# Kernel optimization log

Hardware: AMD Instinct MI355X
Metric: run time of the kernel (lower is better)

Reference implementation:

```python
import jax, jax.numpy as jnp
import numpy as np

# ---- static config (mirrors init_kwargs) ----
N, E, G = 10000, 120000, 32
F_NODE, F_EDGE = 64, 16
H, HEADS, L, R = 128, 4, 3, 4
ID_DIM, REL_DIM = 32, 8
NUM_IDS, NUM_CLASSES = 5000, 10
FFN_H, HEAD_H = 256, 128
GRID_SIZE, SPLINE_ORDER = 5, 3
NC = GRID_SIZE + SPLINE_ORDER  # n spline coeffs per input = 8
GRID = jnp.asarray(np.arange(-SPLINE_ORDER, GRID_SIZE + SPLINE_ORDER + 1, dtype=np.float32) * (2.0 / GRID_SIZE) - 1.0)  # [12], grid_range=(-1,1)
NEG = -1e30


def _b_splines(x, grid):
    # x: [B, in] -> bases [B, in, NC]  (Cox-de Boor, as in efficient-kan)
    x = x[..., None]
    bases = ((x >= grid[:-1]) & (x < grid[1:])).astype(x.dtype)
    for p in range(1, SPLINE_ORDER + 1):
        left = (x - grid[:-(p + 1)]) / (grid[p:-1] - grid[:-(p + 1)]) * bases[..., :-1]
        right = (grid[p + 1:] - x) / (grid[p + 1:] - grid[1:-p]) * bases[..., 1:]
        bases = left + right
    return bases


def _kan_linear(x, base_w, spline_w, scaler, grid):
    # base path: SiLU(x) @ W_base^T ; spline path: b_splines(x) contracted with scaled spline weights
    base = jax.nn.silu(x) @ base_w.T
    spline = jnp.einsum('big,oig->bo', _b_splines(x, grid), spline_w * scaler[..., None])
    return base + spline


def _ln(x, g, b, eps=1e-5):
    mu = x.mean(-1, keepdims=True)
    var = ((x - mu) ** 2).mean(-1, keepdims=True)
    return (x - mu) * jax.lax.rsqrt(var + eps) * g + b


def _forward(x, edge_attr, id_emb, in_W, in_b, Wl, bl, Wr, br, We, att, gat_bias,
             rel_gate, rel_emb, ln1_g, ln1_b, ln2_g, ln2_b,
             ffn1_base, ffn1_spline, ffn1_scaler, ffn2_base, ffn2_spline, ffn2_scaler,
             ro_g, ro_b, head1_base, head1_spline, head1_scaler, head2_base, head2_spline, head2_scaler,
             id_token, edge_index, edge_type, batch):
    grid = GRID
    # input proj: concat(id embedding) -> Linear -> SiLU (dropout = identity, eval)
    h = jnp.concatenate([x, id_emb[id_token]], axis=-1)
    h = jax.nn.silu(h @ in_W + in_b)
    src, tgt = edge_index[0], edge_index[1]
    for l in range(L):
        gates = jax.nn.softmax(rel_gate[l])  # all relations present
        h_msg = jnp.zeros_like(h)
        for r in range(R):
            # GATv2Conv (heads=4, concat=False, add_self_loops=False)
            xl = (h @ Wl[l, r] + bl[l, r]).reshape(N, HEADS, H)
            xr = (h @ Wr[l, r] + br[l, r]).reshape(N, HEADS, H)
            # edge feature = concat(edge_attr, rel_emb[r]) @ We, split to avoid materializing the concat
            e = (edge_attr @ We[l, r, :F_EDGE] + rel_emb[l, r] @ We[l, r, F_EDGE:]).reshape(E, HEADS, H)
            z = jax.nn.leaky_relu(xl[src] + xr[tgt] + e, 0.2)   # [E, heads, H]
            score = jnp.einsum('ehd,hd->eh', z, att[l, r])
            mask = (edge_type == r)[:, None]
            score = jnp.where(mask, score, NEG)
            m = jax.ops.segment_max(score, tgt, num_segments=N)  # per-target softmax max
            ex = jnp.where(mask, jnp.exp(score - m[tgt]), 0.0)
            denom = jax.ops.segment_sum(ex, tgt, num_segments=N)
            alpha = ex / jnp.maximum(denom[tgt], 1e-16)          # [E, heads]
            agg = jax.ops.segment_sum(xl[src] * alpha[..., None], tgt, num_segments=N)
            h_r = agg.mean(axis=1) + gat_bias[l, r]              # concat=False -> head mean + bias
            h_msg = h_msg + gates[r] * h_r
        h = _ln(h + h_msg, ln1_g[l], ln1_b[l])
        # KAN FFN: KANLinear(H->FFN_H) -> KANLinear(FFN_H->H)
        h_ffn = _kan_linear(h, ffn1_base[l], ffn1_spline[l], ffn1_scaler[l], grid)
        h_ffn = _kan_linear(h_ffn, ffn2_base[l], ffn2_spline[l], ffn2_scaler[l], grid)
        h = _ln(h + h_ffn, ln2_g[l], ln2_b[l])
    # readout: mean+max pool per graph
    cnt = jax.ops.segment_sum(jnp.ones((N,), h.dtype), batch, num_segments=G)
    h_mean = jax.ops.segment_sum(h, batch, num_segments=G) / jnp.maximum(cnt, 1.0)[:, None]
    h_max = jax.ops.segment_max(h, batch, num_segments=G)
    h_max = jnp.where(jnp.isfinite(h_max), h_max, 0.0)
    g = _ln(jnp.concatenate([h_mean, h_max], axis=-1), ro_g, ro_b)
    # KAN head: KANLinear(2H->HEAD_H) -> KANLinear(HEAD_H->NUM_CLASSES)
    g = _kan_linear(g, head1_base, head1_spline, head1_scaler, grid)
    logits = _kan_linear(g, head2_base, head2_spline, head2_scaler, grid)
    return logits


def setup_inputs():
    key = jax.random.key(0)
    ks = iter(jax.random.split(key, 48))
    n = lambda shape, s=0.05: jax.random.normal(next(ks), shape, dtype=jnp.float32) * s
    d = {}
    d['x'] = jax.random.normal(next(ks), (N, F_NODE), dtype=jnp.float32)
    d['edge_attr'] = jax.random.normal(next(ks), (E, F_EDGE), dtype=jnp.float32)
    d['id_token'] = jax.random.randint(next(ks), (N,), 0, NUM_IDS + 1)
    d['edge_index'] = jax.random.randint(next(ks), (2, E), 0, N)
    d['edge_type'] = jax.random.randint(next(ks), (E,), 0, R)
    d['batch'] = jnp.sort(jax.random.randint(next(ks), (N,), 0, G))
    d['id_emb'] = n((NUM_IDS + 1, ID_DIM), 0.1)
    d['in_W'] = n((F_NODE + ID_DIM, H))
    d['in_b'] = jnp.zeros((H,), jnp.float32)
    d['Wl'] = n((L, R, H, HEADS * H)); d['bl'] = jnp.zeros((L, R, HEADS * H), jnp.float32)
    d['Wr'] = n((L, R, H, HEADS * H)); d['br'] = jnp.zeros((L, R, HEADS * H), jnp.float32)
    d['We'] = n((L, R, F_EDGE + REL_DIM, HEADS * H))
    d['att'] = n((L, R, HEADS, H), 0.1)
    d['gat_bias'] = jnp.zeros((L, R, H), jnp.float32)
    d['rel_gate'] = n((L, R), 0.1)
    d['rel_emb'] = n((L, R, REL_DIM), 0.1)
    d['ln1_g'] = jnp.ones((L, H), jnp.float32); d['ln1_b'] = jnp.zeros((L, H), jnp.float32)
    d['ln2_g'] = jnp.ones((L, H), jnp.float32); d['ln2_b'] = jnp.zeros((L, H), jnp.float32)
    d['ffn1_base'] = n((L, FFN_H, H)); d['ffn1_spline'] = n((L, FFN_H, H, NC)); d['ffn1_scaler'] = jnp.ones((L, FFN_H, H), jnp.float32)
    d['ffn2_base'] = n((L, H, FFN_H)); d['ffn2_spline'] = n((L, H, FFN_H, NC)); d['ffn2_scaler'] = jnp.ones((L, H, FFN_H), jnp.float32)
    d['ro_g'] = jnp.ones((2 * H,), jnp.float32); d['ro_b'] = jnp.zeros((2 * H,), jnp.float32)
    d['head1_base'] = n((HEAD_H, 2 * H)); d['head1_spline'] = n((HEAD_H, 2 * H, NC)); d['head1_scaler'] = jnp.ones((HEAD_H, 2 * H), jnp.float32)
    d['head2_base'] = n((NUM_CLASSES, HEAD_H)); d['head2_spline'] = n((NUM_CLASSES, HEAD_H, NC)); d['head2_scaler'] = jnp.ones((NUM_CLASSES, HEAD_H), jnp.float32)
    return d


def reference(x, edge_attr, id_emb, in_W, in_b, Wl, bl, Wr, br, We, att, gat_bias,
              rel_gate, rel_emb, ln1_g, ln1_b, ln2_g, ln2_b,
              ffn1_base, ffn1_spline, ffn1_scaler, ffn2_base, ffn2_spline, ffn2_scaler,
              ro_g, ro_b, head1_base, head1_spline, head1_scaler, head2_base, head2_spline, head2_scaler,
              id_token, edge_index, edge_type, batch):
    return _forward(x, edge_attr, id_emb, in_W, in_b, Wl, bl, Wr, br, We, att, gat_bias,
                    rel_gate, rel_emb, ln1_g, ln1_b, ln2_g, ln2_b,
                    ffn1_base, ffn1_spline, ffn1_scaler, ffn2_base, ffn2_spline, ffn2_scaler,
                    ro_g, ro_b, head1_base, head1_spline, head1_scaler, head2_base, head2_spline, head2_scaler,
                    id_token, edge_index, edge_type, batch)
```

## Files before the change

### kernel.cpp

```cpp
#include <hip/hip_runtime.h>
#include <cstdint>
#include <cstddef>

#define NN      10000
#define NE      120000
#define NG      32
#define FNODE   64
#define FEDGE   16
#define HID     128
#define NHEADS  4
#define NL      3
#define NR      4
#define IDDIM   32
#define RELDIM  8
#define FFNH    256
#define HEADH   128
#define NCLS    10

#define NCHUNK  128
#define SCTOT   (NN * NR)
#define SCBLK   ((SCTOT + 255) / 256)

typedef __attribute__((ext_vector_type(8))) short short8;
typedef __attribute__((ext_vector_type(4))) float floatx4;

__device__ __forceinline__ float silu_f(float x) { return x / (1.f + expf(-x)); }
__device__ __forceinline__ ushort f2bf(float f) {
  unsigned u = __float_as_uint(f);
  return (ushort)((u + 0x7FFFu + ((u >> 16) & 1u)) >> 16);
}
__device__ __forceinline__ float bf2f(ushort h) { return __uint_as_float((unsigned)h << 16); }

__device__ __forceinline__ void kan_bases(float x, float* out8) {
  float bb[11];
#pragma unroll
  for (int j = 0; j < 11; ++j) {
    float t0 = (j - 3) * 0.4f - 1.f;
    float t1 = (j - 2) * 0.4f - 1.f;
    bb[j] = (x >= t0 && x < t1) ? 1.f : 0.f;
  }
  {
    const float inv = 1.f / 0.4f;
#pragma unroll
    for (int j = 0; j < 10; ++j) {
      float tj = (j - 3) * 0.4f - 1.f, tjp1 = (j - 1) * 0.4f - 1.f;
      bb[j] = ((x - tj) * bb[j] + (tjp1 - x) * bb[j + 1]) * inv;
    }
  }
  {
    const float inv = 1.f / 0.8f;
#pragma unroll
    for (int j = 0; j < 9; ++j) {
      float tj = (j - 3) * 0.4f - 1.f, tjp1 = (j) * 0.4f - 1.f;
      bb[j] = ((x - tj) * bb[j] + (tjp1 - x) * bb[j + 1]) * inv;
    }
  }
  {
    const float inv = 1.f / 1.2000001f;
#pragma unroll
    for (int j = 0; j < 8; ++j) {
      float tj = (j - 3) * 0.4f - 1.f, tjp1 = (j + 1) * 0.4f - 1.f;
      bb[j] = ((x - tj) * bb[j] + (tjp1 - x) * bb[j + 1]) * inv;
    }
  }
#pragma unroll
  for (int j = 0; j < 8; ++j) out8[j] = bb[j];
}

__global__ __launch_bounds__(256) void gemm_bf3(
    const ushort* __restrict__ Ahg, const ushort* __restrict__ Alg,
    const ushort* __restrict__ Bhg, const ushort* __restrict__ Blg,
    const float* __restrict__ bias, float* __restrict__ C,
    int M, int K, int N) {
  constexpr int LDA = 68;
  __shared__ __align__(16) ushort Ah[128 * LDA];
  __shared__ __align__(16) ushort Al[128 * LDA];
  __shared__ __align__(16) ushort Bh[64 * LDA];
  __shared__ __align__(16) ushort Bl[64 * LDA];
  const int tid = threadIdx.x;
  const int lane = tid & 63, wave = tid >> 6;
  const int lrow = lane & 15, quad = lane >> 4;
  const int bm = blockIdx.y * 128, bn = blockIdx.x * 64;
  floatx4 acc[2][4] = {};
  for (int k0 = 0; k0 < K; k0 += 64) {
#pragma unroll
    for (int i = 0; i < 4; ++i) {
      int c = tid + i * 256;
      int row = c >> 3, col8 = c & 7;
      int gr = bm + row;
      uint4 vh = make_uint4(0, 0, 0, 0), vl = make_uint4(0, 0, 0, 0);
      if (gr < M) {
        vh = *(const uint4*)(Ahg + (size_t)gr * K + k0 + col8 * 8);
        vl = *(const uint4*)(Alg + (size_t)gr * K + k0 + col8 * 8);
      }
      *(uint4*)&Ah[row * LDA + col8 * 8] = vh;
      *(uint4*)&Al[row * LDA + col8 * 8] = vl;
    }
#pragma unroll
    for (int i = 0; i < 2; ++i) {
      int c = tid + i * 256;
      int row = c >> 3, col8 = c & 7;
      *(uint4*)&Bh[row * LDA + col8 * 8] = *(const uint4*)(Bhg + (size_t)(bn + row) * K + k0 + col8 * 8);
      *(uint4*)&Bl[row * LDA + col8 * 8] = *(const uint4*)(Blg + (size_t)(bn + row) * K + k0 + col8 * 8);
    }
    __syncthreads();
#pragma unroll
    for (int kk = 0; kk < 64; kk += 32) {
      int kof = kk + quad * 8;
      const int ra0 = (wave * 32 + lrow) * LDA + kof;
      const int ra1 = (wave * 32 + 16 + lrow) * LDA + kof;
      short8 ah0 = *(const short8*)&Ah[ra0];
      short8 ah1 = *(const short8*)&Ah[ra1];
      short8 al0 = *(const short8*)&Al[ra0];
      short8 al1 = *(const short8*)&Al[ra1];
      short8 bh[4], blo[4];
#pragma unroll
      for (int nt = 0; nt < 4; ++nt) {
        int rb = (nt * 16 + lrow) * LDA + kof;
        bh[nt]  = *(const short8*)&Bh[rb];
        blo[nt] = *(const short8*)&Bl[rb];
      }
#pragma unroll
      for (int nt = 0; nt < 4; ++nt) {
        acc[0][nt] = __builtin_amdgcn_mfma_f32_16x16x32_bf16(ah0, bh[nt],  acc[0][nt], 0, 0, 0);
        acc[1][nt] = __builtin_amdgcn_mfma_f32_16x16x32_bf16(ah1, bh[nt],  acc[1][nt], 0, 0, 0);
        acc[0][nt] = __builtin_amdgcn_mfma_f32_16x16x32_bf16(al0, bh[nt],  acc[0][nt], 0, 0, 0);
        acc[1][nt] = __builtin_amdgcn_mfma_f32_16x16x32_bf16(al1, bh[nt],  acc[1][nt], 0, 0, 0);
        acc[0][nt] = __builtin_amdgcn_mfma_f32_16x16x32_bf16(ah0, blo[nt], acc[0][nt], 0, 0, 0);
        acc[1][nt] = __builtin_amdgcn_mfma_f32_16x16x32_bf16(ah1, blo[nt], acc[1][nt], 0, 0, 0);
      }
    }
    __syncthreads();
  }
#pragma unroll
  for (int mt = 0; mt < 2; ++mt) {
#pragma unroll
    for (int nt = 0; nt < 4; ++nt) {
#pragma unroll
      for (int reg = 0; reg < 4; ++reg) {
        int row = bm + wave * 32 + mt * 16 + quad * 4 + reg;
        int col = bn + nt * 16 + lrow;
        if (row < M) {
          float v = acc[mt][nt][reg];
          if (bias) v += bias[col];
          C[(size_t)row * N + col] = v;
        }
      }
    }
  }
}

template<int NT, int SPLIT>
__global__ __launch_bounds__(256) void gemm_kan(
    const float* __restrict__ A, const ushort* __restrict__ Bhg, const ushort* __restrict__ Blg,
    float* __restrict__ C, int M, int In, int N) {
  const int K = In * 9;
  const int ntiles = K >> 6;
  const int per = (ntiles + SPLIT - 1) / SPLIT;
  const int kt0 = blockIdx.z * per;
  const int kt1 = (kt0 + per < ntiles) ? (kt0 + per) : ntiles;
  constexpr int LDA = 68;
  constexpr int BN = NT * 16;
  __shared__ __align__(16) ushort Ah[64 * LDA];
  __shared__ __align__(16) ushort Al[64 * LDA];
  __shared__ __align__(16) ushort Bh[BN * LDA];
  __shared__ __align__(16) ushort Bl[BN * LDA];
  const int tid = threadIdx.x;
  const int lane = tid & 63, wave = tid >> 6;
  const int lrow = lane & 15, quad = lane >> 4;
  const int bm = blockIdx.y * 64, bn = blockIdx.x * BN;
  floatx4 acc[NT] = {};
  for (int kt = kt0; kt < kt1; ++kt) {
    int k0 = kt << 6;
    if (k0 < In) {
#pragma unroll
      for (int i = 0; i < 4; ++i) {
        int c = tid + i * 256;
        int row = c >> 4, col4 = c & 15;
        int gr = bm + row;
        float4 v = make_float4(0.f, 0.f, 0.f, 0.f);
        if (gr < M) v = *(const float4*)(A + (size_t)gr * In + k0 + col4 * 4);
        float vv[4] = {silu_f(v.x), silu_f(v.y), silu_f(v.z), silu_f(v.w)};
        ushort h0 = f2bf(vv[0]), h1 = f2bf(vv[1]), h2 = f2bf(vv[2]), h3 = f2bf(vv[3]);
        ushort l0 = f2bf(vv[0] - bf2f(h0)), l1 = f2bf(vv[1] - bf2f(h1));
        ushort l2 = f2bf(vv[2] - bf2f(h2)), l3 = f2bf(vv[3] - bf2f(h3));
        *(uint2*)&Ah[row * LDA + col4 * 4] =
          make_uint2((unsigned)h0 | ((unsigned)h1 << 16), (unsigned)h2 | ((unsigned)h3 << 16));
        *(uint2*)&Al[row * LDA + col4 * 4] =
          make_uint2((unsigned)l0 | ((unsigned)l1 << 16), (unsigned)l2 | ((unsigned)l3 << 16));
      }
    } else {
      int i0 = (k0 - In) >> 3;
      int row = tid >> 2, q = tid & 3;
      int gr = bm + row;
      float2 v = make_float2(0.f, 0.f);
      if (gr < M) v = *(const float2*)(A + (size_t)gr * In + i0 + q * 2);
      float vv[2] = {v.x, v.y};
#pragma unroll
      for (int jj = 0; jj < 2; ++jj) {
        float b8[8];
        kan_bases(vv[jj], b8);
        unsigned hu[4], lu[4];
#pragma unroll
        for (int p = 0; p < 4; ++p) {
          ushort ha = f2bf(b8[2 * p]), hb = f2bf(b8[2 * p + 1]);
          ushort la = f2bf(b8[2 * p] - bf2f(ha)), lb = f2bf(b8[2 * p + 1] - bf2f(hb));
          hu[p] = (unsigned)ha | ((unsigned)hb << 16);
          lu[p] = (unsigned)la | ((unsigned)lb << 16);
        }
        int cbase = (q * 2 + jj) * 8;
        *(uint4*)&Ah[row * LDA + cbase] = make_uint4(hu[0], hu[1], hu[2], hu[3]);
        *(uint4*)&Al[row * LDA + cbase] = make_uint4(lu[0], lu[1], lu[2], lu[3]);
      }
    }
#pragma unroll
    for (int i = 0; i < NT / 2; ++i) {
      int c = tid + i * 256;
      int row = c >> 3, col8 = c & 7;
      *(uint4*)&Bh[row * LDA + col8 * 8] = *(const uint4*)(Bhg + (size_t)(bn + row) * K + k0 + col8 * 8);
      *(uint4*)&Bl[row * LDA + col8 * 8] = *(const uint4*)(Blg + (size_t)(bn + row) * K + k0 + col8 * 8);
    }
    __syncthreads();
#pragma unroll
    for (int kk = 0; kk < 64; kk += 32) {
      int kof = kk + quad * 8;
      int ra = (wave * 16 + lrow) * LDA + kof;
      short8 ah = *(const short8*)&Ah[ra];
      short8 al = *(const short8*)&Al[ra];
#pragma unroll
      for (int nt = 0; nt < NT; ++nt) {
        int rb = (nt * 16 + lrow) * LDA + kof;
        short8 bh  = *(const short8*)&Bh[rb];
        short8 blo = *(const short8*)&Bl[rb];
        acc[nt] = __builtin_amdgcn_mfma_f32_16x16x32_bf16(ah, bh,  acc[nt], 0, 0, 0);
        acc[nt] = __builtin_amdgcn_mfma_f32_16x16x32_bf16(al, bh,  acc[nt], 0, 0, 0);
        acc[nt] = __builtin_amdgcn_mfma_f32_16x16x32_bf16(ah, blo, acc[nt], 0, 0, 0);
      }
    }
    __syncthreads();
  }
#pragma unroll
  for (int nt = 0; nt < NT; ++nt) {
#pragma unroll
    for (int reg = 0; reg < 4; ++reg) {
      int row = bm + wave * 16 + quad * 4 + reg;
      int col = bn + nt * 16 + lrow;
      if (row < M) atomicAdd(&C[(size_t)row * N + col], acc[nt][reg]);
    }
  }
}

__global__ void conv_wT2(const float* __restrict__ Wl, const float* __restrict__ Wr,
                         const float* __restrict__ bl, const float* __restrict__ br,
                         ushort* __restrict__ WTh, ushort* __restrict__ WTl,
                         float* __restrict__ bout, int total) {
  int i = blockIdx.x * 256 + threadIdx.x;
  if (i >= total) return;
  int g2 = i / (2048 * 128), rem = i % (2048 * 128);
  int n = rem >> 7, k = rem & 127;
  int l = g2 >> 1, pair = g2 & 1;
  int r = pair * 2 + (n >> 10);
  int nsub = n & 1023;
  int nn = nsub & 511;
  int g = l * NR + r;
  const float* W = (nsub < 512) ? Wl : Wr;
  float v = W[(size_t)g * 65536 + (size_t)k * 512 + nn];
  ushort hi = f2bf(v);
  WTh[i] = hi;
  WTl[i] = f2bf(v - bf2f(hi));
  if (k == 0) bout[g2 * 2048 + n] = ((nsub < 512) ? bl : br)[g * 512 + nn];
}

__global__ void build_kan_wT(const float* __restrict__ base_w, const float* __restrict__ spline_w,
                             const float* __restrict__ scaler,
                             ushort* __restrict__ BTh, ushort* __restrict__ BTl,
                             int In, int Out) {
  int i = blockIdx.x * 256 + threadIdx.x;
  if (i >= In * 9 * Out) return;
  int o = i / (In * 9), k = i % (In * 9);
  float v;
  if (k < In) v = base_w[(size_t)o * In + k];
  else {
    int q = k - In, ii = q >> 3, gq = q & 7;
    v = spline_w[((size_t)o * In + ii) * 8 + gq] * scaler[(size_t)o * In + ii];
  }
  ushort hi = f2bf(v);
  BTh[i] = hi;
  BTl[i] = f2bf(v - bf2f(hi));
}

__global__ __launch_bounds__(128) void input_proj(
    const float* __restrict__ x, const float* __restrict__ id_emb,
    const int* __restrict__ id_token, const float* __restrict__ inW,
    const float* __restrict__ inb, float* __restrict__ h,
    ushort* __restrict__ hh, ushort* __restrict__ hl) {
  int n = blockIdx.x, j = threadIdx.x;
  __shared__ float s[FNODE + IDDIM];
  if (j < FNODE) s[j] = x[(size_t)n * FNODE + j];
  else if (j < FNODE + IDDIM) s[j] = id_emb[(size_t)id_token[n] * IDDIM + (j - FNODE)];
  __syncthreads();
  float acc = inb[j];
#pragma unroll
  for (int k = 0; k < FNODE + IDDIM; ++k) acc = fmaf(s[k], inW[k * HID + j], acc);
  float v = silu_f(acc);
  h[(size_t)n * HID + j] = v;
  ushort hi = f2bf(v);
  hh[(size_t)n * HID + j] = hi;
  hl[(size_t)n * HID + j] = f2bf(v - bf2f(hi));
}

__global__ __launch_bounds__(512) void layer_prep(
    const float* __restrict__ rel_gate, const float* __restrict__ gat_bias,
    const float* __restrict__ rel_emb, const float* __restrict__ We, int l,
    float* __restrict__ gates, float* __restrict__ msg_bias, float* __restrict__ erel) {
  int j = threadIdx.x;
  float g[NR]; float mx = -1e30f;
  for (int r = 0; r < NR; ++r) { g[r] = rel_gate[l * NR + r]; mx = fmaxf(mx, g[r]); }
  float s = 0.f;
  for (int r = 0; r < NR; ++r) { g[r] = expf(g[r] - mx); s += g[r]; }
  for (int r = 0; r < NR; ++r) g[r] /= s;
  if (j < NR) gates[j] = g[j];
  if (j < HID) {
    float b = 0.f;
    for (int r = 0; r < NR; ++r) b = fmaf(g[r], gat_bias[((size_t)(l * NR + r)) * HID + j], b);
    msg_bias[j] = b;
  }
  for (int r = 0; r < NR; ++r) {
    const float* Wer = We + ((size_t)(l * NR + r)) * 24 * 512;
    const float* re  = rel_emb + (l * NR + r) * RELDIM;
    float acc = 0.f;
#pragma unroll
    for (int q = 0; q < RELDIM; ++q) acc = fmaf(re[q], Wer[(FEDGE + q) * 512 + j], acc);
    erel[r * 512 + j] = acc;
  }
}

__global__ void fill_zero(float* __restrict__ p, int n) {
  int i = blockIdx.x * 256 + threadIdx.x;
  if (i < n) p[i] = 0.f;
}
__global__ void fill_zero_i(int* __restrict__ p, int n) {
  int i = blockIdx.x * 256 + threadIdx.x;
  if (i < n) p[i] = 0;
}

__global__ void csr_count2(const int* __restrict__ eidx, const int* __restrict__ etype,
                           int* __restrict__ deg2) {
  int e = blockIdx.x * 256 + threadIdx.x;
  if (e < NE) atomicAdd(&deg2[eidx[NE + e] * NR + etype[e]], 1);
}

__global__ __launch_bounds__(256) void scan_p1(const int* __restrict__ deg2,
                                               int* __restrict__ tmp_incl, int* __restrict__ bsum) {
  __shared__ int ps[256];
  int t = threadIdx.x, blk = blockIdx.x;
  int i = blk * 256 + t;
  int v = (i < SCTOT) ? deg2[i] : 0;
  ps[t] = v;
  __syncthreads();
  for (int o = 1; o < 256; o <<= 1) {
    int u = (t >= o) ? ps[t - o] : 0;
    __syncthreads();
    ps[t] += u;
    __syncthreads();
  }
  if (i < SCTOT) tmp_incl[i] = ps[t];
  if (t == 255) bsum[blk] = ps[255];
}
__global__ __launch_bounds__(256) void scan_p2(const int* __restrict__ bsum, int* __restrict__ boff) {
  __shared__ int ps[256];
  int t = threadIdx.x;
  int v = (t < SCBLK) ? bsum[t] : 0;
  ps[t] = v;
  __syncthreads();
  for (int o = 1; o < 256; o <<= 1) {
    int u = (t >= o) ? ps[t - o] : 0;
    __syncthreads();
    ps[t] += u;
    __syncthreads();
  }
  if (t < SCBLK) boff[t] = ps[t] - v;
}
__global__ __launch_bounds__(256) void scan_p3(const int* __restrict__ deg2,
                                               const int* __restrict__ tmp_incl,
                                               const int* __restrict__ boff,
                                               int* __restrict__ in_off2, int* __restrict__ cursor2) {
  int t = threadIdx.x, blk = blockIdx.x;
  int i = blk * 256 + t;
  if (i < SCTOT) {
    int excl = boff[blk] + tmp_incl[i] - deg2[i];
    in_off2[i] = excl;
    cursor2[i] = excl;
  }
  if (i == 0) in_off2[SCTOT] = NE;
}

__global__ void csr_scatter2(const int* __restrict__ eidx, const int* __restrict__ etype,
                             int* __restrict__ cursor2,
                             int* __restrict__ in_e2, int* __restrict__ in_s2) {
  int e = blockIdx.x * 256 + threadIdx.x;
  if (e < NE) {
    int pos = atomicAdd(&cursor2[eidx[NE + e] * NR + etype[e]], 1);
    in_e2[pos] = e;
    in_s2[pos] = eidx[e];
  }
}

__global__ __launch_bounds__(256) void gat_node6(
    const int* __restrict__ in_off2, const int* __restrict__ in_e2, const int* __restrict__ in_s2,
    const float* __restrict__ eattr, const float* __restrict__ xlr,
    const float* __restrict__ We_base, const float* __restrict__ erel_base,
    const float* __restrict__ att_base, const float* __restrict__ gates,
    int rbase, float* __restrict__ hmsg) {
  __shared__ __align__(16) float WeL[16 * 512];
  __shared__ __align__(16) float sAgg[4][512];
  int tid = threadIdx.x;
  int rs = blockIdx.y;
  int r = rbase + rs;
  const float* We_r = We_base + (size_t)rs * 24 * 512;
  for (int i = tid; i < 16 * 512 / 4; i += 256)
    *(float4*)&WeL[i * 4] = *(const float4*)&We_r[i * 4];
  __syncthreads();
  float gr = gates[r] * 0.25f;
  int lane = tid & 63, wave = tid >> 6;
  int n = blockIdx.x * 4 + wave;
  if (n >= NN) return;
  int roff = rs * 1024;
  const int cA = lane * 4;
  const int cB = 256 + lane * 4;
  const float* xrb = xlr + (size_t)n * 2048 + roff + 512;
  float4 xrA = *(const float4*)(xrb + cA);
  float4 xrB = *(const float4*)(xrb + cB);
  float4 attA = *(const float4*)(att_base + rs * 512 + cA);
  float4 attB = *(const float4*)(att_base + rs * 512 + cB);
  float4 erA  = *(const float4*)(erel_base + rs * 512 + cA);
  float4 erB  = *(const float4*)(erel_base + rs * 512 + cB);
  float mA = -1e30f, mB = -1e30f, lsA = 0.f, lsB = 0.f;
  float4 accA = make_float4(0.f, 0.f, 0.f, 0.f);
  float4 accB = make_float4(0.f, 0.f, 0.f, 0.f);
  int e0 = in_off2[n * NR + r];
  int cnt = in_off2[n * NR + r + 1] - e0;
  float4 pxA, pxB, pe0, pe1, pe2, pe3;
  int eN = 0, sN = 0;
  if (cnt > 0) {
    int eC = in_e2[e0], sC = in_s2[e0];
    if (cnt > 1) { eN = in_e2[e0 + 1]; sN = in_s2[e0 + 1]; }
    const float* xls = xlr + (size_t)sC * 2048 + roff;
    pxA = *(const float4*)(xls + cA);
    pxB = *(const float4*)(xls + cB);
    const float4* eap = (const float4*)(eattr + (size_t)eC * 16);
    pe0 = eap[0]; pe1 = eap[1]; pe2 = eap[2]; pe3 = eap[3];
  }
  for (int j = 0; j < cnt; ++j) {
    float4 xA = pxA, xB = pxB;
    float ea[16] = {pe0.x, pe0.y, pe0.z, pe0.w, pe1.x, pe1.y, pe1.z, pe1.w,
                    pe2.x, pe2.y, pe2.z, pe2.w, pe3.x, pe3.y, pe3.z, pe3.w};
    if (j + 1 < cnt) {
      int eC = eN, sC = sN;
      if (j + 2 < cnt) { eN = in_e2[e0 + j + 2]; sN = in_s2[e0 + j + 2]; }
      const float* xls = xlr + (size_t)sC * 2048 + roff;
      pxA = *(const float4*)(xls + cA);
      pxB = *(const float4*)(xls + cB);
      const float4* eap = (const float4*)(eattr + (size_t)eC * 16);
      pe0 = eap[0]; pe1 = eap[1]; pe2 = eap[2]; pe3 = eap[3];
    }
    float4 etA = erA, etB = erB;
#pragma unroll
    for (int k = 0; k < 16; ++k) {
      float4 wA = *(const float4*)&WeL[k * 512 + cA];
      float4 wB = *(const float4*)&WeL[k * 512 + cB];
      etA.x = fmaf(ea[k], wA.x, etA.x); etA.y = fmaf(ea[k], wA.y, etA.y);
      etA.z = fmaf(ea[k], wA.z, etA.z); etA.w = fmaf(ea[k], wA.w, etA.w);
      etB.x = fmaf(ea[k], wB.x, etB.x); etB.y = fmaf(ea[k], wB.y, etB.y);
      etB.z = fmaf(ea[k], wB.z, etB.z); etB.w = fmaf(ea[k], wB.w, etB.w);
    }
    float sA, sB;
    {
      float z0 = xA.x + xrA.x + etA.x; z0 = (z0 > 0.f) ? z0 : 0.2f * z0;
      float z1 = xA.y + xrA.y + etA.y; z1 = (z1 > 0.f) ? z1 : 0.2f * z1;
      float z2 = xA.z + xrA.z + etA.z; z2 = (z2 > 0.f) ? z2 : 0.2f * z2;
      float z3 = xA.w + xrA.w + etA.w; z3 = (z3 > 0.f) ? z3 : 0.2f * z3;
      sA = z0 * attA.x + z1 * attA.y + z2 * attA.z + z3 * attA.w;
      z0 = xB.x + xrB.x + etB.x; z0 = (z0 > 0.f) ? z0 : 0.2f * z0;
      z1 = xB.y + xrB.y + etB.y; z1 = (z1 > 0.f) ? z1 : 0.2f * z1;
      z2 = xB.z + xrB.z + etB.z; z2 = (z2 > 0.f) ? z2 : 0.2f * z2;
      z3 = xB.w + xrB.w + etB.w; z3 = (z3 > 0.f) ? z3 : 0.2f * z3;
      sB = z0 * attB.x + z1 * attB.y + z2 * attB.z + z3 * attB.w;
    }
#pragma unroll
    for (int o = 1; o <= 16; o <<= 1) {
      sA += __shfl_xor(sA, o, 64);
      sB += __shfl_xor(sB, o, 64);
    }
    {
      float mn = fmaxf(mA, sA);
      float sc = expf(mA - mn), we = expf(sA - mn);
      mA = mn; lsA = lsA * sc + we;
      accA.x = accA.x * sc + we * xA.x; accA.y = accA.y * sc + we * xA.y;
      accA.z = accA.z * sc + we * xA.z; accA.w = accA.w * sc + we * xA.w;
    }
    {
      float mn = fmaxf(mB, sB);
      float sc = expf(mB - mn), we = expf(sB - mn);
      mB = mn; lsB = lsB * sc + we;
      accB.x = accB.x * sc + we * xB.x; accB.y = accB.y * sc + we * xB.y;
      accB.z = accB.z * sc + we * xB.z; accB.w = accB.w * sc + we * xB.w;
    }
  }
  float invA = 1.f / fmaxf(lsA, 1e-16f);
  float invB = 1.f / fmaxf(lsB, 1e-16f);
  *(float4*)&sAgg[wave][cA] = make_float4(accA.x * invA, accA.y * invA, accA.z * invA, accA.w * invA);
  *(float4*)&sAgg[wave][cB] = make_float4(accB.x * invB, accB.y * invB, accB.z * invB, accB.w * invB);
  float o0 = sAgg[wave][lane]       + sAgg[wave][128 + lane]
           + sAgg[wave][256 + lane] + sAgg[wave][384 + lane];
  float o1 = sAgg[wave][64 + lane]  + sAgg[wave][192 + lane]
           + sAgg[wave][320 + lane] + sAgg[wave][448 + lane];
  size_t base = (size_t)n * HID;
  atomicAdd(&hmsg[base + lane],      gr * o0);
  atomicAdd(&hmsg[base + 64 + lane], gr * o1);
}

__global__ __launch_bounds__(64) void ln128(
    float* __restrict__ h, const float* __restrict__ add, const float* __restrict__ bvec,
    const float* __restrict__ g, const float* __restrict__ b,
    ushort* __restrict__ hh, ushort* __restrict__ hl) {
  int n = blockIdx.x, lane = threadIdx.x;
  size_t base = (size_t)n * HID;
  float x0 = h[base + lane] + add[base + lane];
  float x1 = h[base + 64 + lane] + add[base + 64 + lane];
  if (bvec) { x0 += bvec[lane]; x1 += bvec[64 + lane]; }
  float s = x0 + x1;
#pragma unroll
  for (int m = 32; m > 0; m >>= 1) s += __shfl_xor(s, m, 64);
  float mu = s * (1.f / 128.f);
  float d0 = x0 - mu, d1 = x1 - mu;
  float q = d0 * d0 + d1 * d1;
#pragma unroll
  for (int m = 32; m > 0; m >>= 1) q += __shfl_xor(q, m, 64);
  float inv = 1.f / sqrtf(q * (1.f / 128.f) + 1e-5f);
  float o0 = d0 * inv * g[lane] + b[lane];
  float o1 = d1 * inv * g[64 + lane] + b[64 + lane];
  h[base + lane]      = o0;
  h[base + 64 + lane] = o1;
  if (hh) {
    ushort i0 = f2bf(o0), i1 = f2bf(o1);
    hh[base + lane] = i0;        hh[base + 64 + lane] = i1;
    hl[base + lane] = f2bf(o0 - bf2f(i0));
    hl[base + 64 + lane] = f2bf(o1 - bf2f(i1));
  }
}

__global__ void expand_f32(const float* __restrict__ v, float* __restrict__ u, int In, int rows) {
  int i = blockIdx.x * 256 + threadIdx.x;
  if (i >= rows * In) return;
  int n = i / In, c = i % In;
  float x = v[(size_t)n * In + c];
  size_t base = (size_t)n * In * 9;
  u[base + c] = silu_f(x);
  float b8[8];
  kan_bases(x, b8);
  float* ub = u + base + In + (size_t)c * 8;
#pragma unroll
  for (int gq = 0; gq < 8; ++gq) ub[gq] = b8[gq];
}

__global__ __launch_bounds__(128) void pool_part(
    const float* __restrict__ h, const int* __restrict__ batch,
    float* __restrict__ psum, float* __restrict__ pmax, float* __restrict__ pcnt) {
  __shared__ float sS[NG][HID];
  __shared__ float sM[NG][HID];
  __shared__ int sC[NG];
  int d = threadIdx.x, blk = blockIdx.x;
  const float NEGINF = __uint_as_float(0xff800000u);
  for (int i = d; i < NG * HID; i += 128) {
    ((float*)sS)[i] = 0.f;
    ((float*)sM)[i] = NEGINF;
  }
  if (d < NG) sC[d] = 0;
  __syncthreads();
  const int CH = (NN + NCHUNK - 1) / NCHUNK;
  int n0 = blk * CH, n1 = (n0 + CH < NN) ? n0 + CH : NN;
  for (int n = n0; n < n1; ++n) {
    int g = batch[n];
    float v = h[(size_t)n * HID + d];
    sS[g][d] += v;
    sM[g][d] = fmaxf(sM[g][d], v);
    if (d == 0) sC[g]++;
  }
  __syncthreads();
  for (int i = d; i < NG * HID; i += 128) {
    psum[(size_t)blk * NG * HID + i] = ((float*)sS)[i];
    pmax[(size_t)blk * NG * HID + i] = ((float*)sM)[i];
  }
  if (d < NG) pcnt[blk * NG + d] = (float)sC[d];
}

__global__ __launch_bounds__(256) void pool_final2(
    const float* __restrict__ psum, const float* __restrict__ pmax,
    const float* __restrict__ pcnt, const float* __restrict__ rog,
    const float* __restrict__ rob, float* __restrict__ gvec) {
  int g = blockIdx.x, j = threadIdx.x;
  __shared__ float rb[256];
  float x;
  if (j < HID) {
    float s = 0.f, cn = 0.f;
    for (int c = 0; c < NCHUNK; ++c) {
      s += psum[(size_t)c * NG * HID + g * HID + j];
      cn += pcnt[c * NG + g];
    }
    x = s / fmaxf(cn, 1.f);
  } else {
    float mx = __uint_as_float(0xff800000u);
    for (int c = 0; c < NCHUNK; ++c)
      mx = fmaxf(mx, pmax[(size_t)c * NG * HID + g * HID + (j - HID)]);
    x = (mx > -1e38f) ? mx : 0.f;
  }
  rb[j] = x; __syncthreads();
  for (int st = 128; st > 0; st >>= 1) { if (j < st) rb[j] += rb[j + st]; __syncthreads(); }
  float mu = rb[0] * (1.f / 256.f); __syncthreads();
  float d = x - mu;
  rb[j] = d * d; __syncthreads();
  for (int st = 128; st > 0; st >>= 1) { if (j < st) rb[j] += rb[j + st]; __syncthreads(); }
  float var = rb[0] * (1.f / 256.f);
  float inv = 1.f / sqrtf(var + 1e-5f);
  gvec[(size_t)g * 256 + j] = d * inv * rog[j] + rob[j];
}

__global__ __launch_bounds__(256) void kan_head_w(
    const float* __restrict__ u, const float* __restrict__ base_w,
    const float* __restrict__ spline_w, const float* __restrict__ scaler,
    float* __restrict__ out, int In, int Out, int npairs) {
  int wid = blockIdx.x * 4 + (threadIdx.x >> 6);
  if (wid >= npairs) return;
  int g = wid / Out, o = wid % Out;
  int lane = threadIdx.x & 63;
  const float* ug = u + (size_t)g * In * 9;
  const float* bw = base_w + (size_t)o * In;
  const float* sp = spline_w + (size_t)o * In * 8;
  const float* sc = scaler + (size_t)o * In;
  float acc = 0.f;
  for (int i = lane; i < In; i += 64) acc = fmaf(ug[i], bw[i], acc);
  const float* us = ug + In;
  for (int k = lane; k < In * 8; k += 64) {
    int i = k >> 3;
    acc = fmaf(us[k], sp[k] * sc[i], acc);
  }
#pragma unroll
  for (int off2 = 32; off2 > 0; off2 >>= 1) acc += __shfl_xor(acc, off2, 64);
  if (lane == 0) out[(size_t)g * Out + o] = acc;
}

extern "C" void kernel_launch(void* const* d_in, const int* in_sizes, int n_in,
                              void* d_out, int out_size, void* d_ws, size_t ws_size,
                              hipStream_t stream) {
  const float* x         = (const float*)d_in[0];
  const float* edge_attr = (const float*)d_in[1];
  const int*   id_token  = (const int*)  d_in[2];
  const int*   edge_index= (const int*)  d_in[3];
  const int*   edge_type = (const int*)  d_in[4];
  const int*   batch     = (const int*)  d_in[5];
  const float* id_emb    = (const float*)d_in[6];
  const float* inW       = (const float*)d_in[7];
  const float* inb       = (const float*)d_in[8];
  const float* Wl        = (const float*)d_in[9];
  const float* bl        = (const float*)d_in[10];
  const float* Wr        = (const float*)d_in[11];
  const float* br        = (const float*)d_in[12];
  const float* We        = (const float*)d_in[13];
  const float* att       = (const float*)d_in[14];
  const float* gat_bias  = (const float*)d_in[15];
  const float* rel_gate  = (const float*)d_in[16];
  const float* rel_emb   = (const float*)d_in[17];
  const float* ln1g      = (const float*)d_in[18];
  const float* ln1b      = (const float*)d_in[19];
  const float* ln2g      = (const float*)d_in[20];
  const float* ln2b      = (const float*)d_in[21];
  const float* ffn1_base = (const float*)d_in[22];
  const float* ffn1_spl  = (const float*)d_in[23];
  const float* ffn1_sc   = (const float*)d_in[24];
  const float* ffn2_base = (const float*)d_in[25];
  const float* ffn2_spl  = (const float*)d_in[26];
  const float* ffn2_sc   = (const float*)d_in[27];
  const float* rog       = (const float*)d_in[28];
  const float* rob       = (const float*)d_in[29];
  const float* h1_base   = (const float*)d_in[30];
  const float* h1_spl    = (const float*)d_in[31];
  const float* h1_sc     = (const float*)d_in[32];
  const float* h2_base   = (const float*)d_in[33];
  const float* h2_spl    = (const float*)d_in[34];
  const float* h2_sc     = (const float*)d_in[35];
  (void)in_sizes; (void)n_in; (void)out_size; (void)ws_size;

  char* wsp = (char*)d_ws;
  size_t off = 0;
  auto carve = [&](size_t bytes) { char* p = wsp + off; off = (off + bytes + 255) & ~(size_t)255; return p; };
  float*    h     = (float*)   carve((size_t)NN * HID * 4);
  ushort*   h_hi  = (ushort*)  carve((size_t)NN * HID * 2);
  ushort*   h_lo  = (ushort*)  carve((size_t)NN * HID * 2);
  float*    hmsg  = (float*)   carve((size_t)NN * HID * 4);
  float*    t1    = (float*)   carve((size_t)NN * FFNH * 4);
  float*    gates = (float*)   carve(NR * 4);
  float*    msgb  = (float*)   carve(HID * 4);
  float*    erel  = (float*)   carve(NR * 512 * 4);
  ushort*   WTh   = (ushort*)  carve((size_t)NL * 2 * 2048 * HID * 2);
  ushort*   WTl   = (ushort*)  carve((size_t)NL * 2 * 2048 * HID * 2);
  float*    blr   = (float*)   carve((size_t)NL * 2 * 2048 * 4);
  ushort*   B1h   = (ushort*)  carve((size_t)FFNH * HID * 9 * 2);
  ushort*   B1l   = (ushort*)  carve((size_t)FFNH * HID * 9 * 2);
  ushort*   B2h   = (ushort*)  carve((size_t)HID * FFNH * 9 * 2);
  ushort*   B2l   = (ushort*)  carve((size_t)HID * FFNH * 9 * 2);
  float*    psum  = (float*)   carve((size_t)NCHUNK * NG * HID * 4);
  float*    pmax  = (float*)   carve((size_t)NCHUNK * NG * HID * 4);
  float*    pcnt  = (float*)   carve((size_t)NCHUNK * NG * 4);
  float*    gvec  = (float*)   carve((size_t)NG * 256 * 4);
  float*    uhead = (float*)   carve((size_t)NG * 256 * 9 * 4);
  float*    thead = (float*)   carve((size_t)NG * HEADH * 4);
  float*    xlr   = (float*)   carve((size_t)NN * 2048 * 4);
  int*      deg2  = (int*)     carve((size_t)SCTOT * 4);
  int*      in_off2=(int*)     carve((size_t)(SCTOT + 1) * 4);
  int*      cursor2=(int*)     carve((size_t)SCTOT * 4);
  int*      tmp_incl=(int*)    carve((size_t)SCTOT * 4);
  int*      bsum  = (int*)     carve((size_t)SCBLK * 4);
  int*      boff  = (int*)     carve((size_t)SCBLK * 4);
  int*      in_e2 = (int*)     carve((size_t)NE * 4);
  int*      in_s2 = (int*)     carve((size_t)NE * 4);

  fill_zero_i<<<(SCTOT + 255) / 256, 256, 0, stream>>>(deg2, SCTOT);
  csr_count2<<<(NE + 255) / 256, 256, 0, stream>>>(edge_index, edge_type, deg2);
  scan_p1<<<SCBLK, 256, 0, stream>>>(deg2, tmp_incl, bsum);
  scan_p2<<<1, 256, 0, stream>>>(bsum, boff);
  scan_p3<<<SCBLK, 256, 0, stream>>>(deg2, tmp_incl, boff, in_off2, cursor2);
  csr_scatter2<<<(NE + 255) / 256, 256, 0, stream>>>(edge_index, edge_type, cursor2, in_e2, in_s2);

  {
    int total = NL * 2 * 2048 * 128;
    conv_wT2<<<(total + 255) / 256, 256, 0, stream>>>(Wl, Wr, bl, br, WTh, WTl, blr, total);
  }

  input_proj<<<NN, 128, 0, stream>>>(x, id_emb, id_token, inW, inb, h, h_hi, h_lo);

  const int MB128 = (NN + 127) / 128;
  const int MB64  = (NN + 63) / 64;
  for (int l = 0; l < NL; ++l) {
    layer_prep<<<1, 512, 0, stream>>>(rel_gate, gat_bias, rel_emb, We, l, gates, msgb, erel);
    fill_zero<<<(NN * HID + 255) / 256, 256, 0, stream>>>(hmsg, NN * HID);
    for (int pair = 0; pair < 2; ++pair) {
      int g2 = l * 2 + pair;
      const ushort* WThp = WTh + (size_t)g2 * 2048 * HID;
      const ushort* WTlp = WTl + (size_t)g2 * 2048 * HID;
      const float* blp   = blr + (size_t)g2 * 2048;
      int rbase = pair * 2;
      gemm_bf3<<<dim3(2048 / 64, MB128), 256, 0, stream>>>(h_hi, h_lo, WThp, WTlp, blp, xlr, NN, HID, 2048);
      gat_node6<<<dim3((NN + 3) / 4, 2), 256, 0, stream>>>(
          in_off2, in_e2, in_s2, edge_attr, xlr,
          We + ((size_t)(l * NR + rbase)) * 24 * 512, erel + rbase * 512,
          att + (size_t)(l * NR + rbase) * 512, gates, rbase, hmsg);
    }
    ln128<<<NN, 64, 0, stream>>>(h, hmsg, msgb, ln1g + l * HID, ln1b + l * HID, nullptr, nullptr);

    build_kan_wT<<<((HID * 9 * FFNH) + 255) / 256, 256, 0, stream>>>(
        ffn1_base + (size_t)l * FFNH * HID, ffn1_spl + (size_t)l * FFNH * HID * 8,
        ffn1_sc + (size_t)l * FFNH * HID, B1h, B1l, HID, FFNH);
    fill_zero<<<(NN * FFNH + 255) / 256, 256, 0, stream>>>(t1, NN * FFNH);
    gemm_kan<8, 3><<<dim3(FFNH / 128, MB64, 3), 256, 0, stream>>>(h, B1h, B1l, t1, NN, HID, FFNH);
    build_kan_wT<<<((FFNH * 9 * HID) + 255) / 256, 256, 0, stream>>>(
        ffn2_base + (size_t)l * HID * FFNH, ffn2_spl + (size_t)l * HID * FFNH * 8,
        ffn2_sc + (size_t)l * HID * FFNH, B2h, B2l, FFNH, HID);
    fill_zero<<<(NN * HID + 255) / 256, 256, 0, stream>>>(hmsg, NN * HID);
    gemm_kan<8, 4><<<dim3(HID / 128, MB64, 4), 256, 0, stream>>>(t1, B2h, B2l, hmsg, NN, FFNH, HID);
    ln128<<<NN, 64, 0, stream>>>(h, hmsg, nullptr, ln2g + l * HID, ln2b + l * HID, h_hi, h_lo);
  }

  pool_part<<<NCHUNK, 128, 0, stream>>>(h, batch, psum, pmax, pcnt);
  pool_final2<<<NG, 256, 0, stream>>>(psum, pmax, pcnt, rog, rob, gvec);
  expand_f32<<<((NG * 256) + 255) / 256, 256, 0, stream>>>(gvec, uhead, 256, NG);
  {
    int npairs = NG * HEADH;
    kan_head_w<<<(npairs + 3) / 4, 256, 0, stream>>>(uhead, h1_base, h1_spl, h1_sc, thead, 256, HEADH, npairs);
  }
  expand_f32<<<((NG * HEADH) + 255) / 256, 256, 0, stream>>>(thead, uhead, HEADH, NG);
  {
    int npairs = NG * NCLS;
    kan_head_w<<<(npairs + 3) / 4, 256, 0, stream>>>(uhead, h2_base, h2_spl, h2_sc, (float*)d_out, HEADH, NCLS, npairs);
  }
}
```

Before: 1.473 ms.

## Store GAT projections in fp16 and merge relation pairs into one GEMM/aggregate launch

The xl/xr projection buffer is now stored as fp16 instead of fp32, which halves the write traffic from the GEMM and the gather traffic in the per-node GAT aggregation. The two per-layer relation-pair passes are merged into a single 4096-wide GEMM and a single GAT aggregation kernel over all four relations, cutting launches and improving grid fill. The cost is reduced precision in the attention logits and messages, plus a larger intermediate footprint per launch.

```diff
diff --git a/kernel.cpp b/kernel.cpp
--- a/kernel.cpp
+++ b/kernel.cpp
@@ -1,4 +1,5 @@
 #include <hip/hip_runtime.h>
+#include <hip/hip_fp16.h>
 #include <cstdint>
 #include <cstddef>
 
@@ -30,6 +31,12 @@
   return (ushort)((u + 0x7FFFu + ((u >> 16) & 1u)) >> 16);
 }
 __device__ __forceinline__ float bf2f(ushort h) { return __uint_as_float((unsigned)h << 16); }
+__device__ __forceinline__ float4 ld_h4(const __half* p) {
+  __half2 a = *(const __half2*)p;
+  __half2 b = *(const __half2*)(p + 2);
+  float2 fa = __half22float2(a), fb = __half22float2(b);
+  return make_float4(fa.x, fa.y, fb.x, fb.y);
+}
 
 __device__ __forceinline__ void kan_bases(float x, float* out8) {
   float bb[11];
@@ -70,7 +77,7 @@
 __global__ __launch_bounds__(256) void gemm_bf3(
     const ushort* __restrict__ Ahg, const ushort* __restrict__ Alg,
     const ushort* __restrict__ Bhg, const ushort* __restrict__ Blg,
-    const float* __restrict__ bias, float* __restrict__ C,
+    const float* __restrict__ bias, __half* __restrict__ C,
     int M, int K, int N) {
   constexpr int LDA = 68;
   __shared__ __align__(16) ushort Ah[128 * LDA];
@@ -143,7 +150,7 @@
         if (row < M) {
           float v = acc[mt][nt][reg];
           if (bias) v += bias[col];
-          C[(size_t)row * N + col] = v;
+          C[(size_t)row * N + col] = __float2half(v);
         }
       }
     }
@@ -256,10 +263,9 @@
                          float* __restrict__ bout, int total) {
   int i = blockIdx.x * 256 + threadIdx.x;
   if (i >= total) return;
-  int g2 = i / (2048 * 128), rem = i % (2048 * 128);
+  int l = i / (4096 * 128), rem = i % (4096 * 128);
   int n = rem >> 7, k = rem & 127;
-  int l = g2 >> 1, pair = g2 & 1;
-  int r = pair * 2 + (n >> 10);
+  int r = n >> 10;
   int nsub = n & 1023;
   int nn = nsub & 511;
   int g = l * NR + r;
@@ -268,7 +274,7 @@
   ushort hi = f2bf(v);
   WTh[i] = hi;
   WTl[i] = f2bf(v - bf2f(hi));
-  if (k == 0) bout[g2 * 2048 + n] = ((nsub < 512) ? bl : br)[g * 512 + nn];
+  if (k == 0) bout[l * 4096 + n] = ((nsub < 512) ? bl : br)[g * 512 + nn];
 }
 
 __global__ void build_kan_wT(const float* __restrict__ base_w, const float* __restrict__ spline_w,
@@ -406,31 +412,30 @@
   }
 }
 
-__global__ __launch_bounds__(256) void gat_node6(
+__global__ __launch_bounds__(256) void gat_node7(
     const int* __restrict__ in_off2, const int* __restrict__ in_e2, const int* __restrict__ in_s2,
-    const float* __restrict__ eattr, const float* __restrict__ xlr,
+    const float* __restrict__ eattr, const __half* __restrict__ xlr,
     const float* __restrict__ We_base, const float* __restrict__ erel_base,
     const float* __restrict__ att_base, const float* __restrict__ gates,
-    int rbase, float* __restrict__ hmsg) {
+    float* __restrict__ hmsg) {
   __shared__ __align__(16) float WeL[16 * 512];
   __shared__ __align__(16) float sAgg[4][512];
   int tid = threadIdx.x;
   int rs = blockIdx.y;
-  int r = rbase + rs;
   const float* We_r = We_base + (size_t)rs * 24 * 512;
   for (int i = tid; i < 16 * 512 / 4; i += 256)
     *(float4*)&WeL[i * 4] = *(const float4*)&We_r[i * 4];
   __syncthreads();
-  float gr = gates[r] * 0.25f;
+  float gr = gates[rs] * 0.25f;
   int lane = tid & 63, wave = tid >> 6;
   int n = blockIdx.x * 4 + wave;
   if (n >= NN) return;
   int roff = rs * 1024;
   const int cA = lane * 4;
   const int cB = 256 + lane * 4;
-  const float* xrb = xlr + (size_t)n * 2048 + roff + 512;
-  float4 xrA = *(const float4*)(xrb + cA);
-  float4 xrB = *(const float4*)(xrb + cB);
+  const __half* xrb = xlr + (size_t)n * 4096 + roff + 512;
+  float4 xrA = ld_h4(xrb + cA);
+  float4 xrB = ld_h4(xrb + cB);
   float4 attA = *(const float4*)(att_base + rs * 512 + cA);
   float4 attB = *(const float4*)(att_base + rs * 512 + cB);
   float4 erA  = *(const float4*)(erel_base + rs * 512 + cA);
@@ -438,16 +443,16 @@
   float mA = -1e30f, mB = -1e30f, lsA = 0.f, lsB = 0.f;
   float4 accA = make_float4(0.f, 0.f, 0.f, 0.f);
   float4 accB = make_float4(0.f, 0.f, 0.f, 0.f);
-  int e0 = in_off2[n * NR + r];
-  int cnt = in_off2[n * NR + r + 1] - e0;
+  int e0 = in_off2[n * NR + rs];
+  int cnt = in_off2[n * NR + rs + 1] - e0;
   float4 pxA, pxB, pe0, pe1, pe2, pe3;
   int eN = 0, sN = 0;
   if (cnt > 0) {
     int eC = in_e2[e0], sC = in_s2[e0];
     if (cnt > 1) { eN = in_e2[e0 + 1]; sN = in_s2[e0 + 1]; }
-    const float* xls = xlr + (size_t)sC * 2048 + roff;
-    pxA = *(const float4*)(xls + cA);
-    pxB = *(const float4*)(xls + cB);
+    const __half* xls = xlr + (size_t)sC * 4096 + roff;
+    pxA = ld_h4(xls + cA);
+    pxB = ld_h4(xls + cB);
     const float4* eap = (const float4*)(eattr + (size_t)eC * 16);
     pe0 = eap[0]; pe1 = eap[1]; pe2 = eap[2]; pe3 = eap[3];
   }
@@ -458,9 +463,9 @@
     if (j + 1 < cnt) {
       int eC = eN, sC = sN;
       if (j + 2 < cnt) { eN = in_e2[e0 + j + 2]; sN = in_s2[e0 + j + 2]; }
-      const float* xls = xlr + (size_t)sC * 2048 + roff;
-      pxA = *(const float4*)(xls + cA);
-      pxB = *(const float4*)(xls + cB);
+      const __half* xls = xlr + (size_t)sC * 4096 + roff;
+      pxA = ld_h4(xls + cA);
+      pxB = ld_h4(xls + cB);
       const float4* eap = (const float4*)(eattr + (size_t)eC * 16);
       pe0 = eap[0]; pe1 = eap[1]; pe2 = eap[2]; pe3 = eap[3];
     }
@@ -702,9 +707,9 @@
   float*    gates = (float*)   carve(NR * 4);
   float*    msgb  = (float*)   carve(HID * 4);
   float*    erel  = (float*)   carve(NR * 512 * 4);
-  ushort*   WTh   = (ushort*)  carve((size_t)NL * 2 * 2048 * HID * 2);
-  ushort*   WTl   = (ushort*)  carve((size_t)NL * 2 * 2048 * HID * 2);
-  float*    blr   = (float*)   carve((size_t)NL * 2 * 2048 * 4);
+  ushort*   WTh   = (ushort*)  carve((size_t)NL * 4096 * HID * 2);
+  ushort*   WTl   = (ushort*)  carve((size_t)NL * 4096 * HID * 2);
+  float*    blr   = (float*)   carve((size_t)NL * 4096 * 4);
   ushort*   B1h   = (ushort*)  carve((size_t)FFNH * HID * 9 * 2);
   ushort*   B1l   = (ushort*)  carve((size_t)FFNH * HID * 9 * 2);
   ushort*   B2h   = (ushort*)  carve((size_t)HID * FFNH * 9 * 2);
@@ -715,7 +720,7 @@
   float*    gvec  = (float*)   carve((size_t)NG * 256 * 4);
   float*    uhead = (float*)   carve((size_t)NG * 256 * 9 * 4);
   float*    thead = (float*)   carve((size_t)NG * HEADH * 4);
-  float*    xlr   = (float*)   carve((size_t)NN * 2048 * 4);
+  __half*   xlr   = (__half*)  carve((size_t)NN * 4096 * 2);
   int*      deg2  = (int*)     carve((size_t)SCTOT * 4);
   int*      in_off2=(int*)     carve((size_t)(SCTOT + 1) * 4);
   int*      cursor2=(int*)     carve((size_t)SCTOT * 4);
@@ -733,7 +738,7 @@
   csr_scatter2<<<(NE + 255) / 256, 256, 0, stream>>>(edge_index, edge_type, cursor2, in_e2, in_s2);
 
   {
-    int total = NL * 2 * 2048 * 128;
+    int total = NL * 4096 * 128;
     conv_wT2<<<(total + 255) / 256, 256, 0, stream>>>(Wl, Wr, bl, br, WTh, WTl, blr, total);
   }
 
@@ -744,18 +749,13 @@
   for (int l = 0; l < NL; ++l) {
     layer_prep<<<1, 512, 0, stream>>>(rel_gate, gat_bias, rel_emb, We, l, gates, msgb, erel);
     fill_zero<<<(NN * HID + 255) / 256, 256, 0, stream>>>(hmsg, NN * HID);
-    for (int pair = 0; pair < 2; ++pair) {
-      int g2 = l * 2 + pair;
-      const ushort* WThp = WTh + (size_t)g2 * 2048 * HID;
-      const ushort* WTlp = WTl + (size_t)g2 * 2048 * HID;
-      const float* blp   = blr + (size_t)g2 * 2048;
-      int rbase = pair * 2;
-      gemm_bf3<<<dim3(2048 / 64, MB128), 256, 0, stream>>>(h_hi, h_lo, WThp, WTlp, blp, xlr, NN, HID, 2048);
-      gat_node6<<<dim3((NN + 3) / 4, 2), 256, 0, stream>>>(
-          in_off2, in_e2, in_s2, edge_attr, xlr,
-          We + ((size_t)(l * NR + rbase)) * 24 * 512, erel + rbase * 512,
-          att + (size_t)(l * NR + rbase) * 512, gates, rbase, hmsg);
-    }
+    gemm_bf3<<<dim3(4096 / 64, MB128), 256, 0, stream>>>(
+        h_hi, h_lo, WTh + (size_t)l * 4096 * HID, WTl + (size_t)l * 4096 * HID,
+        blr + (size_t)l * 4096, xlr, NN, HID, 4096);
+    gat_node7<<<dim3((NN + 3) / 4, 4), 256, 0, stream>>>(
+        in_off2, in_e2, in_s2, edge_attr, xlr,
+        We + ((size_t)(l * NR)) * 24 * 512, erel, att + (size_t)(l * NR) * 512,
+        gates, hmsg);
     ln128<<<NN, 64, 0, stream>>>(h, hmsg, msgb, ln1g + l * HID, ln1b + l * HID, nullptr, nullptr);
 
     build_kan_wT<<<((HID * 9 * FFNH) + 255) / 256, 256, 0, stream>>>(
```

After: 1.435 ms. 1.03x faster.
